# Kernel tuning notes

Measured on AMD Instinct MI355X. Metric: run time of the kernel, lower is better.

## Reference

```python
import jax, jax.numpy as jnp
import numpy as np

DIM = 1024
NUM_HEADS = 8
HEAD_DIM = 64
INNER = NUM_HEADS * HEAD_DIM  # 512


def setup_inputs() -> dict:
    key = jax.random.key(0)
    ks = jax.random.split(key, 7)
    B, N, M = 8, 512, 4096
    x = jax.random.normal(ks[0], (B, N, DIM), dtype=jnp.float32)
    context = jax.random.normal(ks[1], (B, M, DIM), dtype=jnp.float32)
    s_in = 1.0 / np.sqrt(DIM)
    s_inner = 1.0 / np.sqrt(INNER)
    # Linear weights stored as [in, out] for x @ W
    Wq = jax.random.normal(ks[2], (DIM, INNER), dtype=jnp.float32) * s_in
    Wk = jax.random.normal(ks[3], (DIM, INNER), dtype=jnp.float32) * s_in
    Wv = jax.random.normal(ks[4], (DIM, INNER), dtype=jnp.float32) * s_in
    Wo = jax.random.normal(ks[5], (INNER, DIM), dtype=jnp.float32) * s_inner
    bo = jax.random.normal(ks[6], (DIM,), dtype=jnp.float32) * 0.01
    return {"x": x, "context": context, "Wq": Wq, "Wk": Wk, "Wv": Wv, "Wo": Wo, "bo": bo}


def reference(x, context, Wq, Wk, Wv, Wo, bo):
    B, N, _ = x.shape
    M = context.shape[1]
    scale = HEAD_DIM ** -0.5
    # project and split heads: [B, H, N, D]
    q = (x @ Wq).reshape(B, N, NUM_HEADS, HEAD_DIM).transpose(0, 2, 1, 3)
    k = (context @ Wk).reshape(B, M, NUM_HEADS, HEAD_DIM).transpose(0, 2, 1, 3)
    v = (context @ Wv).reshape(B, M, NUM_HEADS, HEAD_DIM).transpose(0, 2, 1, 3)
    # full attention matrix [B, H, N, M] as in the original module
    attn = jax.nn.softmax(jnp.einsum('bhnd,bhmd->bhnm', q, k) * scale, axis=-1)
    out = jnp.einsum('bhnm,bhmd->bhnd', attn, v)  # [B, H, N, D]
    out = out.transpose(0, 2, 1, 3).reshape(B, N, INNER)
    return out @ Wo + bo
```

## Files before the change

kernel.cpp:

```cpp
#include <hip/hip_runtime.h>
#include <hip/hip_bf16.h>

#define B_SZ 8
#define N_Q 512
#define M_KV 4096
#define DIM 1024
#define INNER 512
#define NHEADS 8
#define HDIM 64

typedef __attribute__((ext_vector_type(4))) float floatx4;
typedef __attribute__((ext_vector_type(8))) short shortx8;
typedef __attribute__((ext_vector_type(4))) short shortx4;

__device__ inline unsigned short f2bf(float f) {
  union { float f; unsigned u; } x; x.f = f;
  unsigned r = x.u + 0x7FFFu + ((x.u >> 16) & 1u);
  return (unsigned short)(r >> 16);
}

__device__ inline void gload16(const void* g, void* l) {
  __builtin_amdgcn_global_load_lds(
      (const __attribute__((address_space(1))) void*)g,
      (__attribute__((address_space(3))) void*)l, 16, 0, 0);
}

__global__ void k_transpose_bf16(const float* __restrict__ W,
                                 unsigned short* __restrict__ Wt,
                                 int K, int N) {
  int idx = blockIdx.x * 256 + threadIdx.x;
  if (idx >= K * N) return;
  int n = idx / K, k = idx - n * K;
  Wt[idx] = f2bf(W[(long)k * N + n]);
}

template<int MODE, bool ABF, int NCOL, int MBITS>
__global__ __launch_bounds__(512, 4)
void k_gemm(const void* __restrict__ Ap, const unsigned short* __restrict__ Bt,
            void* __restrict__ Cout, void* __restrict__ Cout2,
            const float* __restrict__ bias, int M, int N, int K, float oscale) {
  __shared__ unsigned short As[2][128 * 32];
  __shared__ unsigned short Bs[2][256 * 32];
  const int tid = threadIdx.x;
  const int lane = tid & 63;
  const int w = tid >> 6;
  const int wr = w >> 2, wc = w & 3;

  const int cpx = gridDim.x >> 3;
  const int L = (blockIdx.x & 7) * cpx + (blockIdx.x >> 3);
  const long arow0 = (long)(L / NCOL) * 128;
  const long bcol0 = (long)(L % NCOL) * 256;

  const float* Af = (const float*)Ap;
  const unsigned short* Ah = (const unsigned short*)Ap;

  const int lsub = lane >> 2;
  const int lchunk = (lane & 3) ^ (lsub & 3);
  const long brow0 = bcol0 + (w * 2 + 0) * 16 + lsub;
  const long brow1 = bcol0 + (w * 2 + 1) * 16 + lsub;
  const long ahrow = arow0 + w * 16 + lsub;
  const int arow = tid >> 2;
  const int acseg = tid & 3;
  const int aswz = arow * 32 + ((acseg ^ (arow & 3)) * 8);

  floatx4 acc[4][4] = {};

  #define STAGE_B(buf, kt)                                                   \
    {                                                                        \
      gload16(Bt + brow0 * K + (kt) + lchunk * 8, &Bs[buf][(w * 2) * 512]);  \
      gload16(Bt + brow1 * K + (kt) + lchunk * 8,                            \
              &Bs[buf][(w * 2 + 1) * 512]);                                  \
    }
  #define STAGE_AH(buf, kt) \
    gload16(Ah + ahrow * K + (kt) + lchunk * 8, &As[buf][w * 512]);

  if (ABF) {
    STAGE_AH(0, 0);
  } else {
    const float* src = Af + (arow0 + arow) * (long)K + acseg * 8;
    floatx4 a0 = *reinterpret_cast<const floatx4*>(src);
    floatx4 a1 = *reinterpret_cast<const floatx4*>(src + 4);
    shortx8 h;
    h[0] = (short)f2bf(a0[0]); h[1] = (short)f2bf(a0[1]);
    h[2] = (short)f2bf(a0[2]); h[3] = (short)f2bf(a0[3]);
    h[4] = (short)f2bf(a1[0]); h[5] = (short)f2bf(a1[1]);
    h[6] = (short)f2bf(a1[2]); h[7] = (short)f2bf(a1[3]);
    *reinterpret_cast<shortx8*>(&As[0][aswz]) = h;
  }
  STAGE_B(0, 0);
  __syncthreads();

  const int NK = K >> 5;
  for (int i = 0; i < NK; ++i) {
    const int cur = i & 1;
    const bool more = (i + 1) < NK;
    floatx4 a0, a1;
    if (more) {
      const long ktn = (long)(i + 1) << 5;
      STAGE_B(cur ^ 1, ktn);
      if (ABF) {
        STAGE_AH(cur ^ 1, ktn);
      } else {
        const float* src = Af + (arow0 + arow) * (long)K + ktn + acseg * 8;
        a0 = *reinterpret_cast<const floatx4*>(src);
        a1 = *reinterpret_cast<const floatx4*>(src + 4);
      }
    }

    shortx8 af[4], bf[4];
    #pragma unroll
    for (int rb = 0; rb < 4; ++rb) {
      int row = wr * 64 + rb * 16 + (lane & 15);
      af[rb] = *reinterpret_cast<const shortx8*>(
          &As[cur][row * 32 + (((lane >> 4) ^ (row & 3)) * 8)]);
    }
    #pragma unroll
    for (int cb = 0; cb < 4; ++cb) {
      int row = wc * 64 + cb * 16 + (lane & 15);
      bf[cb] = *reinterpret_cast<const shortx8*>(
          &Bs[cur][row * 32 + (((lane >> 4) ^ (row & 3)) * 8)]);
    }
    #pragma unroll
    for (int rb = 0; rb < 4; ++rb) {
      #pragma unroll
      for (int cb = 0; cb < 4; ++cb)
        acc[rb][cb] = __builtin_amdgcn_mfma_f32_16x16x32_bf16(
            af[rb], bf[cb], acc[rb][cb], 0, 0, 0);
    }

    if (more && !ABF) {
      shortx8 h;
      h[0] = (short)f2bf(a0[0]); h[1] = (short)f2bf(a0[1]);
      h[2] = (short)f2bf(a0[2]); h[3] = (short)f2bf(a0[3]);
      h[4] = (short)f2bf(a1[0]); h[5] = (short)f2bf(a1[1]);
      h[6] = (short)f2bf(a1[2]); h[7] = (short)f2bf(a1[3]);
      *reinterpret_cast<shortx8*>(&As[cur ^ 1][aswz]) = h;
    }
    __syncthreads();
  }
  #undef STAGE_B
  #undef STAGE_AH

  #pragma unroll
  for (int rb = 0; rb < 4; ++rb) {
    #pragma unroll
    for (int cb = 0; cb < 4; ++cb) {
      long gr0 = arow0 + wr * 64 + rb * 16 + (lane >> 4) * 4;
      long gc  = bcol0 + wc * 64 + cb * 16 + (lane & 15);
      if (MODE == 0) {
        float bv = bias[gc];
        #pragma unroll
        for (int r = 0; r < 4; ++r)
          ((float*)Cout)[(gr0 + r) * N + gc] = acc[rb][cb][r] + bv;
      } else if (MODE == 2) {
        long b = gr0 >> MBITS, m = gr0 & ((1 << MBITS) - 1);
        long h = gc >> 6, d = gc & 63;
        #pragma unroll
        for (int r = 0; r < 4; ++r)
          ((unsigned short*)Cout)[((((b * 8 + h) << MBITS) + m + r) << 6) + d] =
              f2bf(acc[rb][cb][r] * oscale);
      } else {
        long b = gr0 >> 12, m = gr0 & 4095;
        if (gc < 512) {
          long h = gc >> 6, d = gc & 63;
          #pragma unroll
          for (int r = 0; r < 4; ++r)
            ((unsigned short*)Cout)[((((b * 8 + h) << 12) + m + r) << 6) + d] =
                f2bf(acc[rb][cb][r]);
        } else {
          long h = (gc - 512) >> 6, d = (gc - 512) & 63;
          shortx4 hv;
          #pragma unroll
          for (int r = 0; r < 4; ++r) hv[r] = (short)f2bf(acc[rb][cb][r]);
          *reinterpret_cast<shortx4*>(
              &((unsigned short*)Cout2)[(((b * 8 + h) * 64 + d) << 12) + m]) = hv;
        }
      }
    }
  }
}

__global__ __launch_bounds__(256, 2)
void k_attn(const unsigned short* __restrict__ Qh,
            const unsigned short* __restrict__ Kh,
            const unsigned short* __restrict__ Vt,
            unsigned short* __restrict__ Aout) {
  __shared__ unsigned short Ks[64][72];
  __shared__ unsigned short Vs[64][72];
  __shared__ unsigned short QPs[64][72];
  const int tid = threadIdx.x;
  const int lane = tid & 63;
  const int w = tid >> 6;
  const int wg = blockIdx.x;
  const int bh = wg & 63;
  const int qt = wg >> 6;
  const int b = bh >> 3, h = bh & 7;

  const unsigned short* Qbase = Qh + (((long)bh << 9) + qt * 64) * 64;
  const unsigned short* Kbase = Kh + (((long)bh) << 18);
  const unsigned short* Vbase = Vt + (((long)bh) << 18);

  const int sr = tid >> 2;
  const int sc = (tid & 3) * 16;

  {
    const unsigned short* src = Qbase + sr * 64 + sc;
    *reinterpret_cast<shortx8*>(&QPs[sr][sc]) =
        *reinterpret_cast<const shortx8*>(src);
    *reinterpret_cast<shortx8*>(&QPs[sr][sc + 8]) =
        *reinterpret_cast<const shortx8*>(src + 8);
  }
  {
    const unsigned short* ksrc = Kbase + sr * 64 + sc;
    *reinterpret_cast<shortx8*>(&Ks[sr][sc]) =
        *reinterpret_cast<const shortx8*>(ksrc);
    *reinterpret_cast<shortx8*>(&Ks[sr][sc + 8]) =
        *reinterpret_cast<const shortx8*>(ksrc + 8);
    const unsigned short* vsrc = Vbase + ((long)sr << 12) + sc;
    *reinterpret_cast<shortx8*>(&Vs[sr][sc]) =
        *reinterpret_cast<const shortx8*>(vsrc);
    *reinterpret_cast<shortx8*>(&Vs[sr][sc + 8]) =
        *reinterpret_cast<const shortx8*>(vsrc + 8);
  }
  __syncthreads();

  shortx8 qf[2];
  qf[0] = *reinterpret_cast<const shortx8*>(
      &QPs[w * 16 + (lane & 15)][(lane >> 4) * 8]);
  qf[1] = *reinterpret_cast<const shortx8*>(
      &QPs[w * 16 + (lane & 15)][32 + (lane >> 4) * 8]);

  floatx4 o_acc[4] = {};
  float l_part[4] = {0.f, 0.f, 0.f, 0.f};
  shortx8 kpre[2], vpre[2];

  for (int mt = 0; mt < M_KV / 64; ++mt) {
    if (mt < M_KV / 64 - 1) {
      const unsigned short* ksrc = Kbase + ((mt + 1) * 64 + sr) * 64 + sc;
      kpre[0] = *reinterpret_cast<const shortx8*>(ksrc);
      kpre[1] = *reinterpret_cast<const shortx8*>(ksrc + 8);
      const unsigned short* vsrc = Vbase + ((long)sr << 12) + (mt + 1) * 64 + sc;
      vpre[0] = *reinterpret_cast<const shortx8*>(vsrc);
      vpre[1] = *reinterpret_cast<const shortx8*>(vsrc + 8);
    }

    floatx4 s[4];
    #pragma unroll
    for (int cb = 0; cb < 4; ++cb) {
      shortx8 k0 = *reinterpret_cast<const shortx8*>(
          &Ks[cb * 16 + (lane & 15)][(lane >> 4) * 8]);
      shortx8 k1 = *reinterpret_cast<const shortx8*>(
          &Ks[cb * 16 + (lane & 15)][32 + (lane >> 4) * 8]);
      floatx4 z = {};
      z = __builtin_amdgcn_mfma_f32_16x16x32_bf16(qf[0], k0, z, 0, 0, 0);
      s[cb] = __builtin_amdgcn_mfma_f32_16x16x32_bf16(qf[1], k1, z, 0, 0, 0);
    }

    #pragma unroll
    for (int cb = 0; cb < 4; ++cb) {
      #pragma unroll
      for (int r = 0; r < 4; ++r) {
        float pv = __expf(s[cb][r]);
        l_part[r] += pv;
        QPs[w * 16 + (lane >> 4) * 4 + r][cb * 16 + (lane & 15)] = f2bf(pv);
      }
    }

    #pragma unroll
    for (int kk = 0; kk < 2; ++kk) {
      shortx8 pf = *reinterpret_cast<const shortx8*>(
          &QPs[w * 16 + (lane & 15)][kk * 32 + (lane >> 4) * 8]);
      #pragma unroll
      for (int db = 0; db < 4; ++db) {
        shortx8 vf = *reinterpret_cast<const shortx8*>(
            &Vs[db * 16 + (lane & 15)][kk * 32 + (lane >> 4) * 8]);
        o_acc[db] = __builtin_amdgcn_mfma_f32_16x16x32_bf16(
            pf, vf, o_acc[db], 0, 0, 0);
      }
    }

    __syncthreads();
    if (mt < M_KV / 64 - 1) {
      *reinterpret_cast<shortx8*>(&Ks[sr][sc]) = kpre[0];
      *reinterpret_cast<shortx8*>(&Ks[sr][sc + 8]) = kpre[1];
      *reinterpret_cast<shortx8*>(&Vs[sr][sc]) = vpre[0];
      *reinterpret_cast<shortx8*>(&Vs[sr][sc + 8]) = vpre[1];
      __syncthreads();
    }
  }

  float inv[4];
  #pragma unroll
  for (int r = 0; r < 4; ++r) {
    float l = l_part[r];
    l += __shfl_xor(l, 1);
    l += __shfl_xor(l, 2);
    l += __shfl_xor(l, 4);
    l += __shfl_xor(l, 8);
    inv[r] = 1.f / l;
  }
  #pragma unroll
  for (int db = 0; db < 4; ++db) {
    #pragma unroll
    for (int r = 0; r < 4; ++r) {
      int n = qt * 64 + w * 16 + (lane >> 4) * 4 + r;
      long idx = ((long)(b * N_Q + n)) * INNER + h * HDIM + db * 16 + (lane & 15);
      Aout[idx] = f2bf(o_acc[db][r] * inv[r]);
    }
  }
}

extern "C" void kernel_launch(void* const* d_in, const int* in_sizes, int n_in,
                              void* d_out, int out_size, void* d_ws, size_t ws_size,
                              hipStream_t stream) {
  const float* x   = (const float*)d_in[0];
  const float* ctx = (const float*)d_in[1];
  const float* Wq  = (const float*)d_in[2];
  const float* Wk  = (const float*)d_in[3];
  const float* Wv  = (const float*)d_in[4];
  const float* Wo  = (const float*)d_in[5];
  const float* bo  = (const float*)d_in[6];
  float* out = (float*)d_out;

  char* ws = (char*)d_ws;
  unsigned short* Qh   = (unsigned short*)(ws);
  unsigned short* Kh   = (unsigned short*)(ws + (4ull  << 20));
  unsigned short* Vt   = (unsigned short*)(ws + (36ull << 20));
  unsigned short* Aat  = (unsigned short*)(ws + (68ull << 20));
  unsigned short* Wqt  = (unsigned short*)(ws + (72ull << 20));
  unsigned short* Wkvt = (unsigned short*)(ws + (73ull << 20));
  unsigned short* Wot  = (unsigned short*)(ws + (75ull << 20));

  k_transpose_bf16<<<(DIM * INNER + 255) / 256, 256, 0, stream>>>(Wq, Wqt, DIM, INNER);
  k_transpose_bf16<<<(DIM * INNER + 255) / 256, 256, 0, stream>>>(Wk, Wkvt, DIM, INNER);
  k_transpose_bf16<<<(DIM * INNER + 255) / 256, 256, 0, stream>>>(
      Wv, Wkvt + (size_t)INNER * DIM, DIM, INNER);
  k_transpose_bf16<<<(INNER * DIM + 255) / 256, 256, 0, stream>>>(Wo, Wot, INNER, DIM);

  dim3 blk(512);
  k_gemm<2, false, 2, 9><<<dim3(64), blk, 0, stream>>>(
      x, Wqt, Qh, nullptr, nullptr, B_SZ * N_Q, INNER, DIM, 0.125f);
  k_gemm<4, false, 4, 12><<<dim3(1024), blk, 0, stream>>>(
      ctx, Wkvt, Kh, Vt, nullptr, B_SZ * M_KV, 2 * INNER, DIM, 1.0f);

  k_attn<<<dim3(B_SZ * NHEADS * (N_Q / 64)), dim3(256), 0, stream>>>(Qh, Kh, Vt, Aat);

  k_gemm<0, true, 4, 0><<<dim3(128), blk, 0, stream>>>(
      Aat, Wot, out, nullptr, bo, B_SZ * N_Q, DIM, INNER, 1.0f);
}
```

Baseline: 230.7 us.

## Add dedicated K/V projection GEMM with 256x256 tiles and pre-swizzled weights

Replaces the generic 128x256 GEMM for the context K/V projection with a specialized kernel using 256x256 tiles and a K-step of 64. The kernel reads weights from a new pre-swizzled buffer so each B tile loads as contiguous 16-byte chunks, and it interleaves the fp32-to-bf16 conversion of context rows across the MFMA phases, with setprio raised around the MFMAs. The LDS swizzle in the generic GEMM also changes to reduce bank conflicts. This adds a staging kernel and more LDS and registers per block, which lowers occupancy (launch bounds 2).

New measurement: 234.9 us. Within noise of the previous version (+1.8%).

```diff
diff --git a/kernel.cpp b/kernel.cpp
--- a/kernel.cpp
+++ b/kernel.cpp
@@ -25,6 +25,13 @@
       (__attribute__((address_space(3))) void*)l, 16, 0, 0);
 }
 
+#define BAR()                                            \
+  do {                                                   \
+    asm volatile("s_waitcnt lgkmcnt(0)" ::: "memory");   \
+    __builtin_amdgcn_s_barrier();                        \
+    asm volatile("" ::: "memory");                       \
+  } while (0)
+
 __global__ void k_transpose_bf16(const float* __restrict__ W,
                                  unsigned short* __restrict__ Wt,
                                  int K, int N) {
@@ -32,6 +39,178 @@
   if (idx >= K * N) return;
   int n = idx / K, k = idx - n * K;
   Wt[idx] = f2bf(W[(long)k * N + n]);
+}
+
+__global__ void k_stage_wkv(const unsigned short* __restrict__ Wkvt,
+                            unsigned short* __restrict__ WkvS) {
+  int idx = blockIdx.x * 256 + threadIdx.x;
+  int nt = idx >> 15;
+  int kt = (idx >> 11) & 15;
+  int ww = idx & 2047;
+  int row = ww >> 3, pos = ww & 7;
+  int c = pos ^ (row & 7);
+  const unsigned short* src = Wkvt + ((long)(nt * 256 + row)) * 1024 + kt * 64 + c * 8;
+  *reinterpret_cast<shortx8*>(&WkvS[(long)idx * 8]) =
+      *reinterpret_cast<const shortx8*>(src);
+}
+
+__global__ __launch_bounds__(512, 2)
+void k_gemm_kv(const float* __restrict__ Actx,
+               const unsigned short* __restrict__ WkvS,
+               unsigned short* __restrict__ Kh,
+               unsigned short* __restrict__ Vt) {
+  __shared__ unsigned short As[2][16384];
+  __shared__ unsigned short Bs[2][16384];
+  const int tid = threadIdx.x;
+  const int lane = tid & 63;
+  const int w = tid >> 6;
+  const int wr = w >> 2, wc = w & 3;
+  const int fr = lane & 15;
+  const int fc = lane >> 4;
+
+  const int L = ((blockIdx.x & 7) << 6) + (blockIdx.x >> 3);
+  const int mt = L >> 2, nt = L & 3;
+  const long arow0 = (long)mt << 8;
+
+  const unsigned short* Bsrc = WkvS + ((long)nt << 18);
+  const int arow_lo = tid >> 3;
+  const int acoff = ((tid & 7) ^ ((tid >> 3) & 7)) << 3;
+  const int ldsA_w0 = (tid << 3);
+
+  floatx4 acc[8][4] = {};
+
+  {
+    #pragma unroll
+    for (int j = 0; j < 4; ++j)
+      gload16(Bsrc + (((j * 512 + tid)) << 3),
+              &Bs[0][(j * 512 + (w << 6)) << 3]);
+    floatx4 a[8];
+    #pragma unroll
+    for (int j = 0; j < 4; ++j) {
+      const float* s = Actx + (arow0 + j * 64 + arow_lo) * 1024 + acoff;
+      a[j * 2] = *reinterpret_cast<const floatx4*>(s);
+      a[j * 2 + 1] = *reinterpret_cast<const floatx4*>(s + 4);
+    }
+    #pragma unroll
+    for (int j = 0; j < 4; ++j) {
+      shortx8 h;
+      h[0] = (short)f2bf(a[j * 2][0]); h[1] = (short)f2bf(a[j * 2][1]);
+      h[2] = (short)f2bf(a[j * 2][2]); h[3] = (short)f2bf(a[j * 2][3]);
+      h[4] = (short)f2bf(a[j * 2 + 1][0]); h[5] = (short)f2bf(a[j * 2 + 1][1]);
+      h[6] = (short)f2bf(a[j * 2 + 1][2]); h[7] = (short)f2bf(a[j * 2 + 1][3]);
+      *reinterpret_cast<shortx8*>(&As[0][(j * 512 + tid) << 3]) = h;
+    }
+  }
+  BAR();
+
+  for (int t = 0; t < 16; ++t) {
+    const int cur = t & 1;
+    const bool more = t < 15;
+    floatx4 a0[4], a1[4];
+    if (more) {
+      const unsigned short* bs = Bsrc + ((long)(t + 1) << 14);
+      #pragma unroll
+      for (int j = 0; j < 4; ++j)
+        gload16(bs + ((j * 512 + tid) << 3),
+                &Bs[cur ^ 1][(j * 512 + (w << 6)) << 3]);
+      const int kn = (t + 1) << 6;
+      #pragma unroll
+      for (int j = 0; j < 2; ++j) {
+        const float* s = Actx + (arow0 + j * 64 + arow_lo) * 1024 + kn + acoff;
+        a0[j * 2] = *reinterpret_cast<const floatx4*>(s);
+        a0[j * 2 + 1] = *reinterpret_cast<const floatx4*>(s + 4);
+      }
+    }
+
+    shortx8 bf[4][2];
+    #pragma unroll
+    for (int nf = 0; nf < 4; ++nf) {
+      const int r = wc * 64 + nf * 16 + fr;
+      #pragma unroll
+      for (int ks = 0; ks < 2; ++ks)
+        bf[nf][ks] = *reinterpret_cast<const shortx8*>(
+            &Bs[cur][r * 64 + (((ks * 4 + fc) ^ (r & 7)) << 3)]);
+    }
+
+    #pragma unroll
+    for (int p = 0; p < 4; ++p) {
+      shortx8 af[2][2];
+      #pragma unroll
+      for (int i = 0; i < 2; ++i) {
+        const int r = wr * 128 + (p * 2 + i) * 16 + fr;
+        #pragma unroll
+        for (int ks = 0; ks < 2; ++ks)
+          af[i][ks] = *reinterpret_cast<const shortx8*>(
+              &As[cur][r * 64 + (((ks * 4 + fc) ^ (r & 7)) << 3)]);
+      }
+      __builtin_amdgcn_s_setprio(1);
+      #pragma unroll
+      for (int i = 0; i < 2; ++i) {
+        #pragma unroll
+        for (int nf = 0; nf < 4; ++nf) {
+          #pragma unroll
+          for (int ks = 0; ks < 2; ++ks)
+            acc[p * 2 + i][nf] = __builtin_amdgcn_mfma_f32_16x16x32_bf16(
+                af[i][ks], bf[nf][ks], acc[p * 2 + i][nf], 0, 0, 0);
+        }
+      }
+      __builtin_amdgcn_s_setprio(0);
+
+      if (more && p == 1) {
+        #pragma unroll
+        for (int j = 0; j < 2; ++j) {
+          shortx8 h;
+          h[0] = (short)f2bf(a0[j * 2][0]); h[1] = (short)f2bf(a0[j * 2][1]);
+          h[2] = (short)f2bf(a0[j * 2][2]); h[3] = (short)f2bf(a0[j * 2][3]);
+          h[4] = (short)f2bf(a0[j * 2 + 1][0]); h[5] = (short)f2bf(a0[j * 2 + 1][1]);
+          h[6] = (short)f2bf(a0[j * 2 + 1][2]); h[7] = (short)f2bf(a0[j * 2 + 1][3]);
+          *reinterpret_cast<shortx8*>(&As[cur ^ 1][(j * 512 + tid) << 3]) = h;
+        }
+        const int kn = (t + 1) << 6;
+        #pragma unroll
+        for (int j = 2; j < 4; ++j) {
+          const float* s = Actx + (arow0 + j * 64 + arow_lo) * 1024 + kn + acoff;
+          a1[(j - 2) * 2] = *reinterpret_cast<const floatx4*>(s);
+          a1[(j - 2) * 2 + 1] = *reinterpret_cast<const floatx4*>(s + 4);
+        }
+      }
+      if (more && p == 3) {
+        #pragma unroll
+        for (int j = 2; j < 4; ++j) {
+          const int i0 = (j - 2) * 2;
+          shortx8 h;
+          h[0] = (short)f2bf(a1[i0][0]); h[1] = (short)f2bf(a1[i0][1]);
+          h[2] = (short)f2bf(a1[i0][2]); h[3] = (short)f2bf(a1[i0][3]);
+          h[4] = (short)f2bf(a1[i0 + 1][0]); h[5] = (short)f2bf(a1[i0 + 1][1]);
+          h[6] = (short)f2bf(a1[i0 + 1][2]); h[7] = (short)f2bf(a1[i0 + 1][3]);
+          *reinterpret_cast<shortx8*>(&As[cur ^ 1][(j * 512 + tid) << 3]) = h;
+        }
+      }
+    }
+    BAR();
+  }
+
+  #pragma unroll
+  for (int mf = 0; mf < 8; ++mf) {
+    #pragma unroll
+    for (int nf = 0; nf < 4; ++nf) {
+      long gr0 = arow0 + wr * 128 + mf * 16 + fc * 4;
+      long gc = (long)nt * 256 + wc * 64 + nf * 16 + fr;
+      long b = gr0 >> 12, m = gr0 & 4095;
+      if (gc < 512) {
+        long h = gc >> 6, d = gc & 63;
+        #pragma unroll
+        for (int r = 0; r < 4; ++r)
+          Kh[((((b * 8 + h) << 12) + m + r) << 6) + d] = f2bf(acc[mf][nf][r]);
+      } else {
+        long h = (gc - 512) >> 6, d = (gc - 512) & 63;
+        shortx4 hv;
+        #pragma unroll
+        for (int r = 0; r < 4; ++r) hv[r] = (short)f2bf(acc[mf][nf][r]);
+        *reinterpret_cast<shortx4*>(&Vt[(((b * 8 + h) * 64 + d) << 12) + m]) = hv;
+      }
+    }
+  }
 }
 
 template<int MODE, bool ABF, int NCOL, int MBITS>
@@ -55,13 +234,13 @@
   const unsigned short* Ah = (const unsigned short*)Ap;
 
   const int lsub = lane >> 2;
-  const int lchunk = (lane & 3) ^ (lsub & 3);
+  const int lchunk = (lane & 3) ^ ((lane >> 3) & 3);
   const long brow0 = bcol0 + (w * 2 + 0) * 16 + lsub;
   const long brow1 = bcol0 + (w * 2 + 1) * 16 + lsub;
   const long ahrow = arow0 + w * 16 + lsub;
   const int arow = tid >> 2;
   const int acseg = tid & 3;
-  const int aswz = arow * 32 + ((acseg ^ (arow & 3)) * 8);
+  const int aswz = arow * 32 + ((acseg ^ ((arow >> 1) & 3)) * 8);
 
   floatx4 acc[4][4] = {};
 
@@ -112,13 +291,13 @@
     for (int rb = 0; rb < 4; ++rb) {
       int row = wr * 64 + rb * 16 + (lane & 15);
       af[rb] = *reinterpret_cast<const shortx8*>(
-          &As[cur][row * 32 + (((lane >> 4) ^ (row & 3)) * 8)]);
+          &As[cur][row * 32 + (((lane >> 4) ^ ((row >> 1) & 3)) * 8)]);
     }
     #pragma unroll
     for (int cb = 0; cb < 4; ++cb) {
       int row = wc * 64 + cb * 16 + (lane & 15);
       bf[cb] = *reinterpret_cast<const shortx8*>(
-          &Bs[cur][row * 32 + (((lane >> 4) ^ (row & 3)) * 8)]);
+          &Bs[cur][row * 32 + (((lane >> 4) ^ ((row >> 1) & 3)) * 8)]);
     }
     #pragma unroll
     for (int rb = 0; rb < 4; ++rb) {
@@ -159,22 +338,6 @@
         for (int r = 0; r < 4; ++r)
           ((unsigned short*)Cout)[((((b * 8 + h) << MBITS) + m + r) << 6) + d] =
               f2bf(acc[rb][cb][r] * oscale);
-      } else {
-        long b = gr0 >> 12, m = gr0 & 4095;
-        if (gc < 512) {
-          long h = gc >> 6, d = gc & 63;
-          #pragma unroll
-          for (int r = 0; r < 4; ++r)
-            ((unsigned short*)Cout)[((((b * 8 + h) << 12) + m + r) << 6) + d] =
-                f2bf(acc[rb][cb][r]);
-        } else {
-          long h = (gc - 512) >> 6, d = (gc - 512) & 63;
-          shortx4 hv;
-          #pragma unroll
-          for (int r = 0; r < 4; ++r) hv[r] = (short)f2bf(acc[rb][cb][r]);
-          *reinterpret_cast<shortx4*>(
-              &((unsigned short*)Cout2)[(((b * 8 + h) * 64 + d) << 12) + m]) = hv;
-        }
       }
     }
   }
@@ -330,21 +493,22 @@
   unsigned short* Wqt  = (unsigned short*)(ws + (72ull << 20));
   unsigned short* Wkvt = (unsigned short*)(ws + (73ull << 20));
   unsigned short* Wot  = (unsigned short*)(ws + (75ull << 20));
+  unsigned short* WkvS = (unsigned short*)(ws + (76ull << 20));
 
   k_transpose_bf16<<<(DIM * INNER + 255) / 256, 256, 0, stream>>>(Wq, Wqt, DIM, INNER);
   k_transpose_bf16<<<(DIM * INNER + 255) / 256, 256, 0, stream>>>(Wk, Wkvt, DIM, INNER);
   k_transpose_bf16<<<(DIM * INNER + 255) / 256, 256, 0, stream>>>(
       Wv, Wkvt + (size_t)INNER * DIM, DIM, INNER);
   k_transpose_bf16<<<(INNER * DIM + 255) / 256, 256, 0, stream>>>(Wo, Wot, INNER, DIM);
-
-  dim3 blk(512);
-  k_gemm<2, false, 2, 9><<<dim3(64), blk, 0, stream>>>(
+  k_stage_wkv<<<dim3(512), dim3(256), 0, stream>>>(Wkvt, WkvS);
+
+  k_gemm<2, false, 2, 9><<<dim3(64), dim3(512), 0, stream>>>(
       x, Wqt, Qh, nullptr, nullptr, B_SZ * N_Q, INNER, DIM, 0.125f);
-  k_gemm<4, false, 4, 12><<<dim3(1024), blk, 0, stream>>>(
-      ctx, Wkvt, Kh, Vt, nullptr, B_SZ * M_KV, 2 * INNER, DIM, 1.0f);
+
+  k_gemm_kv<<<dim3(512), dim3(512), 0, stream>>>(ctx, WkvS, Kh, Vt);
 
   k_attn<<<dim3(B_SZ * NHEADS * (N_Q / 64)), dim3(256), 0, stream>>>(Qh, Kh, Vt, Aat);
 
-  k_gemm<0, true, 4, 0><<<dim3(128), blk, 0, stream>>>(
+  k_gemm<0, true, 4, 0><<<dim3(128), dim3(512), 0, stream>>>(
       Aat, Wot, out, nullptr, bo, B_SZ * N_Q, DIM, INNER, 1.0f);
 }
```

## Add dedicated KV projection GEMM, tiled weight transpose, and new LDS swizzle

Applied to the files above, without the earlier changes.

Replaces the generic 128x256 KV projection GEMM with a dedicated 256-thread kernel using 128x128 tiles, 2048 blocks, higher occupancy and s_setprio around the MFMA block. Rewrites the weight transpose to go through a shared-memory tile with vector loads and stores, so global accesses are coalesced. Changes the LDS XOR swizzle to use (row>>1)&3, aimed at fewer bank conflicts, and moves the B staging after the A loads. Smaller tiles mean each block reloads more of the weights.

New measurement: 246.9 us. 1.07x slower.

```diff
diff --git a/kernel.cpp b/kernel.cpp
--- a/kernel.cpp
+++ b/kernel.cpp
@@ -19,6 +19,15 @@
   return (unsigned short)(r >> 16);
 }
 
+__device__ inline shortx8 cvt8(floatx4 a, floatx4 b) {
+  shortx8 h;
+  h[0] = (short)f2bf(a[0]); h[1] = (short)f2bf(a[1]);
+  h[2] = (short)f2bf(a[2]); h[3] = (short)f2bf(a[3]);
+  h[4] = (short)f2bf(b[0]); h[5] = (short)f2bf(b[1]);
+  h[6] = (short)f2bf(b[2]); h[7] = (short)f2bf(b[3]);
+  return h;
+}
+
 __device__ inline void gload16(const void* g, void* l) {
   __builtin_amdgcn_global_load_lds(
       (const __attribute__((address_space(1))) void*)g,
@@ -28,17 +37,142 @@
 __global__ void k_transpose_bf16(const float* __restrict__ W,
                                  unsigned short* __restrict__ Wt,
                                  int K, int N) {
-  int idx = blockIdx.x * 256 + threadIdx.x;
-  if (idx >= K * N) return;
-  int n = idx / K, k = idx - n * K;
-  Wt[idx] = f2bf(W[(long)k * N + n]);
+  __shared__ unsigned short t[32][36];
+  const int kt = blockIdx.x * 32, nt = blockIdx.y * 32;
+  const int tr = threadIdx.x >> 3;
+  const int tc = (threadIdx.x & 7) * 4;
+  floatx4 v = *reinterpret_cast<const floatx4*>(&W[(long)(kt + tr) * N + nt + tc]);
+  #pragma unroll
+  for (int j = 0; j < 4; ++j) t[tr][tc + j] = f2bf(v[j]);
+  __syncthreads();
+  shortx4 o;
+  #pragma unroll
+  for (int j = 0; j < 4; ++j) o[j] = (short)t[tc + j][tr];
+  *reinterpret_cast<shortx4*>(&Wt[(long)(nt + tr) * K + kt + tc]) = o;
+}
+
+__global__ __launch_bounds__(256, 3)
+void k_gemm_kv(const float* __restrict__ Actx,
+               const unsigned short* __restrict__ Wkvt,
+               unsigned short* __restrict__ Kh,
+               unsigned short* __restrict__ Vt) {
+  __shared__ unsigned short As[2][128 * 32];
+  __shared__ unsigned short Bs[2][128 * 32];
+  const int tid = threadIdx.x;
+  const int lane = tid & 63;
+  const int w = tid >> 6;
+  const int wr = w >> 1, wc = w & 1;
+  const int fr = lane & 15, fc = lane >> 4;
+
+  const int L = ((blockIdx.x & 7) << 8) + (blockIdx.x >> 3);
+  const int mt = L >> 3, nt = L & 7;
+  const long arow0 = (long)mt << 7;
+  const long bcol0 = (long)nt << 7;
+
+  const int arow = tid >> 1;
+  const int ahalf = tid & 1;
+  const int aswz = (arow >> 1) & 3;
+  const int as0 = ((2 * ahalf) ^ aswz) * 8;
+  const int as1 = ((2 * ahalf + 1) ^ aswz) * 8;
+  const int brl = lane >> 2;
+  const int bpos = lane & 3;
+
+  floatx4 acc[4][4] = {};
+
+  {
+    const float* s = Actx + (arow0 + arow) * 1024 + ahalf * 16;
+    floatx4 a0 = *reinterpret_cast<const floatx4*>(s);
+    floatx4 a1 = *reinterpret_cast<const floatx4*>(s + 4);
+    floatx4 a2 = *reinterpret_cast<const floatx4*>(s + 8);
+    floatx4 a3 = *reinterpret_cast<const floatx4*>(s + 12);
+    #pragma unroll
+    for (int j = 0; j < 2; ++j) {
+      int row = (w * 2 + j) * 16 + brl;
+      int c = bpos ^ ((row >> 1) & 3);
+      gload16(Wkvt + (bcol0 + row) * 1024 + c * 8, &Bs[0][(w * 2 + j) * 512]);
+    }
+    *reinterpret_cast<shortx8*>(&As[0][arow * 32 + as0]) = cvt8(a0, a1);
+    *reinterpret_cast<shortx8*>(&As[0][arow * 32 + as1]) = cvt8(a2, a3);
+  }
+  __syncthreads();
+
+  for (int i = 0; i < 32; ++i) {
+    const int cur = i & 1;
+    const bool more = i < 31;
+    floatx4 a0, a1, a2, a3;
+    if (more) {
+      const float* s = Actx + (arow0 + arow) * 1024 + (i + 1) * 32 + ahalf * 16;
+      a0 = *reinterpret_cast<const floatx4*>(s);
+      a1 = *reinterpret_cast<const floatx4*>(s + 4);
+      a2 = *reinterpret_cast<const floatx4*>(s + 8);
+      a3 = *reinterpret_cast<const floatx4*>(s + 12);
+      #pragma unroll
+      for (int j = 0; j < 2; ++j) {
+        int row = (w * 2 + j) * 16 + brl;
+        int c = bpos ^ ((row >> 1) & 3);
+        gload16(Wkvt + (bcol0 + row) * 1024 + (i + 1) * 32 + c * 8,
+                &Bs[cur ^ 1][(w * 2 + j) * 512]);
+      }
+    }
+
+    shortx8 af[4], bf[4];
+    #pragma unroll
+    for (int rb = 0; rb < 4; ++rb) {
+      int row = wr * 64 + rb * 16 + fr;
+      af[rb] = *reinterpret_cast<const shortx8*>(
+          &As[cur][row * 32 + ((fc ^ ((row >> 1) & 3)) * 8)]);
+    }
+    #pragma unroll
+    for (int cb = 0; cb < 4; ++cb) {
+      int row = wc * 64 + cb * 16 + fr;
+      bf[cb] = *reinterpret_cast<const shortx8*>(
+          &Bs[cur][row * 32 + ((fc ^ ((row >> 1) & 3)) * 8)]);
+    }
+    __builtin_amdgcn_s_setprio(1);
+    #pragma unroll
+    for (int rb = 0; rb < 4; ++rb) {
+      #pragma unroll
+      for (int cb = 0; cb < 4; ++cb)
+        acc[rb][cb] = __builtin_amdgcn_mfma_f32_16x16x32_bf16(
+            af[rb], bf[cb], acc[rb][cb], 0, 0, 0);
+    }
+    __builtin_amdgcn_s_setprio(0);
+
+    if (more) {
+      *reinterpret_cast<shortx8*>(&As[cur ^ 1][arow * 32 + as0]) = cvt8(a0, a1);
+      *reinterpret_cast<shortx8*>(&As[cur ^ 1][arow * 32 + as1]) = cvt8(a2, a3);
+    }
+    __syncthreads();
+  }
+
+  #pragma unroll
+  for (int rb = 0; rb < 4; ++rb) {
+    #pragma unroll
+    for (int cb = 0; cb < 4; ++cb) {
+      long gr0 = arow0 + wr * 64 + rb * 16 + fc * 4;
+      long gc = bcol0 + wc * 64 + cb * 16 + fr;
+      long b = gr0 >> 12, m = gr0 & 4095;
+      if (gc < 512) {
+        long h = gc >> 6, d = gc & 63;
+        #pragma unroll
+        for (int r = 0; r < 4; ++r)
+          Kh[((((b * 8 + h) << 12) + m + r) << 6) + d] = f2bf(acc[rb][cb][r]);
+      } else {
+        long h = (gc - 512) >> 6, d = (gc - 512) & 63;
+        shortx4 hv;
+        #pragma unroll
+        for (int r = 0; r < 4; ++r) hv[r] = (short)f2bf(acc[rb][cb][r]);
+        *reinterpret_cast<shortx4*>(&Vt[(((b * 8 + h) * 64 + d) << 12) + m]) = hv;
+      }
+    }
+  }
 }
 
 template<int MODE, bool ABF, int NCOL, int MBITS>
 __global__ __launch_bounds__(512, 4)
 void k_gemm(const void* __restrict__ Ap, const unsigned short* __restrict__ Bt,
-            void* __restrict__ Cout, void* __restrict__ Cout2,
-            const float* __restrict__ bias, int M, int N, int K, float oscale) {
+            void* __restrict__ Cout, const float* __restrict__ bias,
+            int M, int N, int K, float oscale) {
   __shared__ unsigned short As[2][128 * 32];
   __shared__ unsigned short Bs[2][256 * 32];
   const int tid = threadIdx.x;
@@ -55,13 +189,13 @@
   const unsigned short* Ah = (const unsigned short*)Ap;
 
   const int lsub = lane >> 2;
-  const int lchunk = (lane & 3) ^ (lsub & 3);
+  const int lchunk = (lane & 3) ^ ((lane >> 3) & 3);
   const long brow0 = bcol0 + (w * 2 + 0) * 16 + lsub;
   const long brow1 = bcol0 + (w * 2 + 1) * 16 + lsub;
   const long ahrow = arow0 + w * 16 + lsub;
   const int arow = tid >> 2;
   const int acseg = tid & 3;
-  const int aswz = arow * 32 + ((acseg ^ (arow & 3)) * 8);
+  const int aswz = arow * 32 + ((acseg ^ ((arow >> 1) & 3)) * 8);
 
   floatx4 acc[4][4] = {};
 
@@ -80,12 +214,7 @@
     const float* src = Af + (arow0 + arow) * (long)K + acseg * 8;
     floatx4 a0 = *reinterpret_cast<const floatx4*>(src);
     floatx4 a1 = *reinterpret_cast<const floatx4*>(src + 4);
-    shortx8 h;
-    h[0] = (short)f2bf(a0[0]); h[1] = (short)f2bf(a0[1]);
-    h[2] = (short)f2bf(a0[2]); h[3] = (short)f2bf(a0[3]);
-    h[4] = (short)f2bf(a1[0]); h[5] = (short)f2bf(a1[1]);
-    h[6] = (short)f2bf(a1[2]); h[7] = (short)f2bf(a1[3]);
-    *reinterpret_cast<shortx8*>(&As[0][aswz]) = h;
+    *reinterpret_cast<shortx8*>(&As[0][aswz]) = cvt8(a0, a1);
   }
   STAGE_B(0, 0);
   __syncthreads();
@@ -97,7 +226,6 @@
     floatx4 a0, a1;
     if (more) {
       const long ktn = (long)(i + 1) << 5;
-      STAGE_B(cur ^ 1, ktn);
       if (ABF) {
         STAGE_AH(cur ^ 1, ktn);
       } else {
@@ -105,6 +233,7 @@
         a0 = *reinterpret_cast<const floatx4*>(src);
         a1 = *reinterpret_cast<const floatx4*>(src + 4);
       }
+      STAGE_B(cur ^ 1, ktn);
     }
 
     shortx8 af[4], bf[4];
@@ -112,13 +241,13 @@
     for (int rb = 0; rb < 4; ++rb) {
       int row = wr * 64 + rb * 16 + (lane & 15);
       af[rb] = *reinterpret_cast<const shortx8*>(
-          &As[cur][row * 32 + (((lane >> 4) ^ (row & 3)) * 8)]);
+          &As[cur][row * 32 + (((lane >> 4) ^ ((row >> 1) & 3)) * 8)]);
     }
     #pragma unroll
     for (int cb = 0; cb < 4; ++cb) {
       int row = wc * 64 + cb * 16 + (lane & 15);
       bf[cb] = *reinterpret_cast<const shortx8*>(
-          &Bs[cur][row * 32 + (((lane >> 4) ^ (row & 3)) * 8)]);
+          &Bs[cur][row * 32 + (((lane >> 4) ^ ((row >> 1) & 3)) * 8)]);
     }
     #pragma unroll
     for (int rb = 0; rb < 4; ++rb) {
@@ -128,14 +257,8 @@
             af[rb], bf[cb], acc[rb][cb], 0, 0, 0);
     }
 
-    if (more && !ABF) {
-      shortx8 h;
-      h[0] = (short)f2bf(a0[0]); h[1] = (short)f2bf(a0[1]);
-      h[2] = (short)f2bf(a0[2]); h[3] = (short)f2bf(a0[3]);
-      h[4] = (short)f2bf(a1[0]); h[5] = (short)f2bf(a1[1]);
-      h[6] = (short)f2bf(a1[2]); h[7] = (short)f2bf(a1[3]);
-      *reinterpret_cast<shortx8*>(&As[cur ^ 1][aswz]) = h;
-    }
+    if (more && !ABF)
+      *reinterpret_cast<shortx8*>(&As[cur ^ 1][aswz]) = cvt8(a0, a1);
     __syncthreads();
   }
   #undef STAGE_B
@@ -159,22 +282,6 @@
         for (int r = 0; r < 4; ++r)
           ((unsigned short*)Cout)[((((b * 8 + h) << MBITS) + m + r) << 6) + d] =
               f2bf(acc[rb][cb][r] * oscale);
-      } else {
-        long b = gr0 >> 12, m = gr0 & 4095;
-        if (gc < 512) {
-          long h = gc >> 6, d = gc & 63;
-          #pragma unroll
-          for (int r = 0; r < 4; ++r)
-            ((unsigned short*)Cout)[((((b * 8 + h) << 12) + m + r) << 6) + d] =
-                f2bf(acc[rb][cb][r]);
-        } else {
-          long h = (gc - 512) >> 6, d = (gc - 512) & 63;
-          shortx4 hv;
-          #pragma unroll
-          for (int r = 0; r < 4; ++r) hv[r] = (short)f2bf(acc[rb][cb][r]);
-          *reinterpret_cast<shortx4*>(
-              &((unsigned short*)Cout2)[(((b * 8 + h) * 64 + d) << 12) + m]) = hv;
-        }
       }
     }
   }
@@ -331,20 +438,22 @@
   unsigned short* Wkvt = (unsigned short*)(ws + (73ull << 20));
   unsigned short* Wot  = (unsigned short*)(ws + (75ull << 20));
 
-  k_transpose_bf16<<<(DIM * INNER + 255) / 256, 256, 0, stream>>>(Wq, Wqt, DIM, INNER);
-  k_transpose_bf16<<<(DIM * INNER + 255) / 256, 256, 0, stream>>>(Wk, Wkvt, DIM, INNER);
-  k_transpose_bf16<<<(DIM * INNER + 255) / 256, 256, 0, stream>>>(
+  k_transpose_bf16<<<dim3(DIM / 32, INNER / 32), dim3(256), 0, stream>>>(
+      Wq, Wqt, DIM, INNER);
+  k_transpose_bf16<<<dim3(DIM / 32, INNER / 32), dim3(256), 0, stream>>>(
+      Wk, Wkvt, DIM, INNER);
+  k_transpose_bf16<<<dim3(DIM / 32, INNER / 32), dim3(256), 0, stream>>>(
       Wv, Wkvt + (size_t)INNER * DIM, DIM, INNER);
-  k_transpose_bf16<<<(INNER * DIM + 255) / 256, 256, 0, stream>>>(Wo, Wot, INNER, DIM);
-
-  dim3 blk(512);
-  k_gemm<2, false, 2, 9><<<dim3(64), blk, 0, stream>>>(
-      x, Wqt, Qh, nullptr, nullptr, B_SZ * N_Q, INNER, DIM, 0.125f);
-  k_gemm<4, false, 4, 12><<<dim3(1024), blk, 0, stream>>>(
-      ctx, Wkvt, Kh, Vt, nullptr, B_SZ * M_KV, 2 * INNER, DIM, 1.0f);
+  k_transpose_bf16<<<dim3(INNER / 32, DIM / 32), dim3(256), 0, stream>>>(
+      Wo, Wot, INNER, DIM);
+
+  k_gemm<2, false, 2, 9><<<dim3(64), dim3(512), 0, stream>>>(
+      x, Wqt, Qh, nullptr, B_SZ * N_Q, INNER, DIM, 0.125f);
+
+  k_gemm_kv<<<dim3(2048), dim3(256), 0, stream>>>(ctx, Wkvt, Kh, Vt);
 
   k_attn<<<dim3(B_SZ * NHEADS * (N_Q / 64)), dim3(256), 0, stream>>>(Qh, Kh, Vt, Aat);
 
-  k_gemm<0, true, 4, 0><<<dim3(128), blk, 0, stream>>>(
-      Aat, Wot, out, nullptr, bo, B_SZ * N_Q, DIM, INNER, 1.0f);
-}
+  k_gemm<0, true, 4, 0><<<dim3(128), dim3(512), 0, stream>>>(
+      Aat, Wot, out, bo, B_SZ * N_Q, DIM, INNER, 1.0f);
+}
```
